# Kernel tuning notes

Measured on AMD Instinct MI355X. Metric: run time of the kernel, lower is better.

Reference implementation:

```python
import jax, jax.numpy as jnp
import numpy as np

H = 1024          # hidden_size
D = 4             # num_domains
B, S = 8, 2048


def setup_inputs() -> dict:
    key = jax.random.key(0)
    ks = jax.random.split(key, 12)
    inp = {
        "sequence_embeddings": jax.random.normal(ks[0], (B, S, H), jnp.float32),
        "volatility": jax.random.uniform(ks[1], (B, S, 1), jnp.float32) * 0.02 + 0.005,
        "risk_factors": jax.random.normal(ks[2], (B, S, 1), jnp.float32) * 0.01,
        # learned parameters (match torch init scales)
        "domain_feature_weights": jax.random.normal(ks[3], (H, 2 * H), jnp.float32) * 0.02,
        "domain_feature_bias": jnp.zeros((2 * H,), jnp.float32),
        "domain_classifier_weights": jax.random.normal(ks[4], (2 * H, D), jnp.float32) * 0.02,
        "domain_classifier_bias": jnp.zeros((D,), jnp.float32),
        "volatility_router_weights": jax.random.normal(ks[5], (1, 8, D), jnp.float32) * 0.1,
        "volatility_router_bias": jnp.zeros((8, D), jnp.float32),
        "risk_router_weights": jax.random.normal(ks[6], (1, 8, D), jnp.float32) * 0.1,
        "risk_router_bias": jnp.zeros((8, D), jnp.float32),
        "stats_router_weights": jax.random.normal(ks[7], (3, 12, D), jnp.float32) * 0.1,
        "stats_router_bias": jnp.zeros((12, D), jnp.float32),
        "expert_weights": jax.random.normal(ks[8], (D, 2 * H, H), jnp.float32) * 0.02,
        "expert_bias": jnp.zeros((D, H), jnp.float32),
    }
    return inp


def reference(sequence_embeddings, volatility, risk_factors,
              domain_feature_weights, domain_feature_bias,
              domain_classifier_weights, domain_classifier_bias,
              volatility_router_weights, volatility_router_bias,
              risk_router_weights, risk_router_bias,
              stats_router_weights, stats_router_bias,
              expert_weights, expert_bias):
    x = sequence_embeddings
    # shared domain feature extractor: [B,S,H] -> [B,S,2H]
    feat = jnp.tanh(jnp.einsum('bsh,hf->bsf', x, domain_feature_weights) + domain_feature_bias)
    # content-based domain logits [B,S,D]
    dom_logits = jnp.einsum('bsf,fd->bsd', feat, domain_classifier_weights) + domain_classifier_bias
    # volatility router: scalar -> 8 hidden units per domain, tanh, sum -> [B,S,D]
    vol_logits = jnp.tanh(volatility[..., None] * volatility_router_weights[0]
                          + volatility_router_bias).sum(axis=-2)
    # risk router, same structure
    risk_logits = jnp.tanh(risk_factors[..., None] * risk_router_weights[0]
                           + risk_router_bias).sum(axis=-2)
    # per-token statistics (mean/std/max over feature dim) -> [B,S,3]
    stats = jnp.stack([x.mean(axis=-1), x.std(axis=-1), x.max(axis=-1)], axis=-1)
    stats_logits = jnp.tanh(jnp.einsum('bsc,ckd->bskd', stats, stats_router_weights)
                            + stats_router_bias).sum(axis=-2)
    # combined routing distribution over domains
    routing_probs = jax.nn.softmax(dom_logits + vol_logits + risk_logits + stats_logits, axis=-1)
    # dispatch every token through all D experts: [B,S,D,H]
    expert_out = jnp.einsum('bsf,dfh->bsdh', feat, expert_weights) + expert_bias
    # gated combine: [B,S,H]
    out = jnp.einsum('bsd,bsdh->bsh', routing_probs, expert_out)
    return out
```

## Files before the change

kernel.cpp:

```cpp
#include <hip/hip_runtime.h>
#include <hip/hip_bf16.h>
#include <cstdint>
#include <cstddef>

typedef __bf16 bf16_t;
typedef bf16_t bf16x8 __attribute__((ext_vector_type(8)));
typedef bf16_t bf16x4 __attribute__((ext_vector_type(4)));
typedef float  f32x4  __attribute__((ext_vector_type(4)));
typedef int    i32x4  __attribute__((ext_vector_type(4)));

#define TOK 16384
#define Hh  1024
#define F2  2048
#define NC  4096

__device__ __forceinline__ void gload_lds16(const bf16_t* g, bf16_t* lds) {
  __builtin_amdgcn_global_load_lds(
      (const __attribute__((address_space(1))) void*)g,
      (__attribute__((address_space(3))) void*)lds, 16, 0, 0);
}
__device__ __forceinline__ void gload_lds16b(const int8_t* g, int8_t* lds) {
  __builtin_amdgcn_global_load_lds(
      (const __attribute__((address_space(1))) void*)g,
      (__attribute__((address_space(3))) void*)lds, 16, 0, 0);
}

__global__ __launch_bounds__(256)
void k_tr_wf(const float* __restrict__ in, bf16_t* __restrict__ out) {
  __shared__ float T[64][65];
  const int f0 = blockIdx.x * 64, h0 = blockIdx.y * 64;
  const int tid = threadIdx.x;
  const int c4 = (tid & 15) * 4, r = tid >> 4;
  #pragma unroll
  for (int p = 0; p < 4; ++p) {
    int hh = p * 16 + r;
    float4 v = *(const float4*)&in[(size_t)(h0 + hh) * F2 + f0 + c4];
    T[c4 + 0][hh] = v.x; T[c4 + 1][hh] = v.y; T[c4 + 2][hh] = v.z; T[c4 + 3][hh] = v.w;
  }
  __syncthreads();
  #pragma unroll
  for (int p = 0; p < 4; ++p) {
    int ff = p * 16 + r;
    bf16x4 o = { (bf16_t)T[ff][c4 + 0], (bf16_t)T[ff][c4 + 1],
                 (bf16_t)T[ff][c4 + 2], (bf16_t)T[ff][c4 + 3] };
    *(bf16x4*)&out[(size_t)(f0 + ff) * Hh + h0 + c4] = o;
  }
}

__global__ void k_we_scale1(const float* __restrict__ We, float* __restrict__ pmax) {
  int ht = blockIdx.x, fc = blockIdx.y, d = blockIdx.z;
  int h = ht * 256 + threadIdx.x;
  float m = 0.f;
  for (int ff = 0; ff < 256; ++ff) {
    float v = We[((size_t)d * F2 + fc * 256 + ff) * Hh + h];
    m = fmaxf(m, fabsf(v));
  }
  pmax[(size_t)(h * 4 + d) * 8 + fc] = m;
}
__global__ void k_we_scale2(const float* __restrict__ pmax, float* __restrict__ SB) {
  int cp = blockIdx.x * 256 + threadIdx.x;
  float m = 0.f;
  #pragma unroll
  for (int i = 0; i < 8; ++i) m = fmaxf(m, pmax[(size_t)cp * 8 + i]);
  SB[cp] = m;
}

__global__ __launch_bounds__(256)
void k_tr_we(const float* __restrict__ in, const float* __restrict__ SB,
             int8_t* __restrict__ out) {
  __shared__ float T[64][65];
  const int f0 = blockIdx.x * 64, h0 = blockIdx.y * 64, d = blockIdx.z;
  const float* ind = in + (size_t)d * F2 * Hh;
  const int tid = threadIdx.x;
  const int c4 = (tid & 15) * 4, r = tid >> 4;
  #pragma unroll
  for (int p = 0; p < 4; ++p) {
    int ff = p * 16 + r;
    float4 v = *(const float4*)&ind[(size_t)(f0 + ff) * Hh + h0 + c4];
    T[c4 + 0][ff] = v.x; T[c4 + 1][ff] = v.y; T[c4 + 2][ff] = v.z; T[c4 + 3][ff] = v.w;
  }
  __syncthreads();
  #pragma unroll
  for (int p = 0; p < 4; ++p) {
    int hh = p * 16 + r;
    int cp = (h0 + hh) * 4 + d;
    float m = SB[cp];
    float inv = (m > 1e-30f) ? 127.f / m : 0.f;
    char4 o;
    o.x = (int8_t)__float2int_rn(T[hh][c4 + 0] * inv);
    o.y = (int8_t)__float2int_rn(T[hh][c4 + 1] * inv);
    o.z = (int8_t)__float2int_rn(T[hh][c4 + 2] * inv);
    o.w = (int8_t)__float2int_rn(T[hh][c4 + 3] * inv);
    *(char4*)&out[(size_t)cp * F2 + f0 + c4] = o;
  }
}

__global__ void k_router_w(const float* __restrict__ x, const float* __restrict__ vol,
                           const float* __restrict__ risk, const float* __restrict__ clsb,
                           const float* __restrict__ vw, const float* __restrict__ vb,
                           const float* __restrict__ rw, const float* __restrict__ rb,
                           const float* __restrict__ sw, const float* __restrict__ sb,
                           bf16_t* __restrict__ xbf, float* __restrict__ LP,
                           int m0, int Tc) {
  int w = threadIdx.x >> 6, l = threadIdx.x & 63;
  int t = blockIdx.x * 4 + w;
  if (t >= Tc) return;
  int s = m0 + t;
  const float4* xr = (const float4*)(x + (size_t)s * Hh);
  bf16x4* xo = (bf16x4*)(xbf + (size_t)s * Hh);
  float sum = 0.f, sq = 0.f, mx = -1e30f;
  #pragma unroll
  for (int it = 0; it < 4; ++it) {
    float4 v = xr[it * 64 + l];
    sum += v.x + v.y + v.z + v.w;
    sq  += v.x * v.x + v.y * v.y + v.z * v.z + v.w * v.w;
    mx = fmaxf(mx, fmaxf(fmaxf(v.x, v.y), fmaxf(v.z, v.w)));
    bf16x4 o = { (bf16_t)v.x, (bf16_t)v.y, (bf16_t)v.z, (bf16_t)v.w };
    xo[it * 64 + l] = o;
  }
  #pragma unroll
  for (int off = 32; off; off >>= 1) {
    sum += __shfl_xor(sum, off, 64);
    sq  += __shfl_xor(sq,  off, 64);
    mx   = fmaxf(mx, __shfl_xor(mx, off, 64));
  }
  if (l < 4) {
    int d = l;
    float mean = sum * (1.0f / Hh);
    float var  = sq * (1.0f / Hh) - mean * mean;
    float sd   = sqrtf(fmaxf(var, 0.f));
    float v = vol[s], rk = risk[s];
    float acc = clsb[d];
    #pragma unroll
    for (int k = 0; k < 8; ++k)  acc += tanhf(v  * vw[k*4+d] + vb[k*4+d]);
    #pragma unroll
    for (int k = 0; k < 8; ++k)  acc += tanhf(rk * rw[k*4+d] + rb[k*4+d]);
    #pragma unroll
    for (int k = 0; k < 12; ++k)
      acc += tanhf(mean * sw[k*4+d] + sd * sw[48 + k*4+d] + mx * sw[96 + k*4+d] + sb[k*4+d]);
    LP[t * 4 + d] = acc;
  }
}

__global__ void k_dom(const int8_t* __restrict__ feat, const float* __restrict__ Wc,
                      float* __restrict__ LP) {
  int w = threadIdx.x >> 6, l = threadIdx.x & 63;
  int t = blockIdx.x * 4 + w;
  const int8_t* fr = feat + (size_t)t * F2;
  const float4* Wc4 = (const float4*)Wc;
  float a0 = 0, a1 = 0, a2 = 0, a3 = 0;
  #pragma unroll
  for (int it = 0; it < 4; ++it) {
    int f0 = it * 512 + l * 8;
    int2 v = *(const int2*)(fr + f0);
    #pragma unroll
    for (int j = 0; j < 8; ++j) {
      int word = (j < 4) ? v.x : v.y;
      float vf = (float)((signed char)(word >> (8 * (j & 3)))) * (1.f / 127.f);
      float4 wv = Wc4[f0 + j];
      a0 += vf * wv.x; a1 += vf * wv.y; a2 += vf * wv.z; a3 += vf * wv.w;
    }
  }
  #pragma unroll
  for (int off = 32; off; off >>= 1) {
    a0 += __shfl_xor(a0, off, 64); a1 += __shfl_xor(a1, off, 64);
    a2 += __shfl_xor(a2, off, 64); a3 += __shfl_xor(a3, off, 64);
  }
  if (l == 0) {
    float l0 = a0 + LP[t*4+0], l1 = a1 + LP[t*4+1];
    float l2 = a2 + LP[t*4+2], l3 = a3 + LP[t*4+3];
    float m = fmaxf(fmaxf(l0, l1), fmaxf(l2, l3));
    float e0 = expf(l0 - m), e1 = expf(l1 - m), e2 = expf(l2 - m), e3 = expf(l3 - m);
    float inv = 1.f / (e0 + e1 + e2 + e3);
    LP[t*4+0] = e0 * inv; LP[t*4+1] = e1 * inv; LP[t*4+2] = e2 * inv; LP[t*4+3] = e3 * inv;
  }
}

__global__ __launch_bounds__(512, 4)
void k_feat_gemm256(const bf16_t* __restrict__ A, const bf16_t* __restrict__ Bt,
                    const float* __restrict__ bias, int8_t* __restrict__ feat, int nbm) {
  constexpr int K = Hh, NT = K / 32;
  __shared__ bf16_t lds[2 * 8192 + 2 * 4096];
  bf16_t* ldsB = lds + 16384;
  const int tid = threadIdx.x;
  const int l = tid & 63, wid = tid >> 6;
  const int wm = wid >> 1, wn = wid & 1;
  const int l15 = l & 15, lg = l >> 4;

  const int nwg = nbm * 16, cpx = nwg >> 3;
  int swzb = (blockIdx.x & 7) * cpx + (blockIdx.x >> 3);
  const int bm = swzb % nbm, bn = swzb / nbm;

  const bf16_t* gA = A  + (size_t)(bm * 256) * K;
  const bf16_t* gB = Bt + (size_t)(bn * 128) * K;

  int aRow[2], aGx[2];
  #pragma unroll
  for (int i = 0; i < 2; ++i) {
    int slot = i * 512 + tid;
    aRow[i] = slot >> 2;
    aGx[i]  = ((slot & 3) ^ ((aRow[i] >> 1) & 3)) << 3;
  }
  const int bRow = tid >> 2;
  const int bGx  = ((tid & 3) ^ ((bRow >> 1) & 3)) << 3;

  #define STAGE(ts) do {                                                       \
    int b_ = (ts) & 1;                                                         \
    _Pragma("unroll")                                                          \
    for (int i = 0; i < 2; ++i)                                                \
      gload_lds16(gA + (size_t)aRow[i] * K + (ts) * 32 + aGx[i],               \
                  lds + b_ * 8192 + (i * 512 + tid) * 8);                      \
    gload_lds16(gB + (size_t)bRow * K + (ts) * 32 + bGx,                       \
                ldsB + b_ * 4096 + tid * 8);                                   \
  } while (0)
  #define FENCE asm volatile("" ::: "memory")

  const int cswz = ((lg ^ ((l15 >> 1) & 3)) << 3);
  f32x4 acc[4][4] = {};

  STAGE(0);
  asm volatile("s_waitcnt vmcnt(0)" ::: "memory");
  FENCE; __builtin_amdgcn_s_barrier(); FENCE;

  for (int t = 0; t < NT; ++t) {
    const bf16_t* As_ = lds  + (t & 1) * 8192;
    const bf16_t* Bs_ = ldsB + (t & 1) * 4096;
    if (t + 1 < NT) STAGE(t + 1);
    bf16x8 af[4], bf[4];
    #pragma unroll
    for (int ni = 0; ni < 4; ++ni)
      bf[ni] = *(const bf16x8*)&Bs_[(wn * 64 + ni * 16 + l15) * 32 + cswz];
    #pragma unroll
    for (int mi = 0; mi < 4; ++mi)
      af[mi] = *(const bf16x8*)&As_[(wm * 64 + mi * 16 + l15) * 32 + cswz];
    __builtin_amdgcn_s_setprio(1);
    #pragma unroll
    for (int ni = 0; ni < 4; ++ni)
      #pragma unroll
      for (int mi = 0; mi < 4; ++mi)
        acc[mi][ni] = __builtin_amdgcn_mfma_f32_16x16x32_bf16(af[mi], bf[ni], acc[mi][ni], 0, 0, 0);
    __builtin_amdgcn_s_setprio(0);
    asm volatile("s_waitcnt vmcnt(0)" ::: "memory");
    FENCE; __builtin_amdgcn_s_barrier(); FENCE;
  }
  #undef STAGE
  #undef FENCE

  #pragma unroll
  for (int ni = 0; ni < 4; ++ni) {
    int gn = bn * 128 + wn * 64 + ni * 16 + l15;
    float bv = bias[gn];
    #pragma unroll
    for (int mi = 0; mi < 4; ++mi) {
      int gmBase = bm * 256 + wm * 64 + mi * 16 + lg * 4;
      #pragma unroll
      for (int r = 0; r < 4; ++r) {
        float tv = tanhf(acc[mi][ni][r] + bv);
        feat[(size_t)(gmBase + r) * F2 + gn] = (int8_t)__float2int_rn(tv * 127.f);
      }
    }
  }
}

__global__ __launch_bounds__(512, 4)
void k_expert_gemm256(const int8_t* __restrict__ A, const int8_t* __restrict__ Bt,
                      const float* __restrict__ P, const float* __restrict__ EB,
                      const float* __restrict__ SBq, float* __restrict__ out, int nbm) {
  constexpr int K = F2, NT = K / 64;
  __shared__ int8_t lds[2 * 16384 + 2 * 8192];
  int8_t* ldsB = lds + 32768;
  const int tid = threadIdx.x;
  const int l = tid & 63, wid = tid >> 6;
  const int wm = wid >> 1, wn = wid & 1;
  const int l15 = l & 15, lg = l >> 4;

  const int nwg = nbm * 32, cpx = nwg >> 3;
  int swzb = (blockIdx.x & 7) * cpx + (blockIdx.x >> 3);
  const int bm = swzb % nbm, bn = swzb / nbm;

  const int8_t* gA = A  + (size_t)(bm * 256) * K;
  const int8_t* gB = Bt + (size_t)(bn * 128) * K;

  int aRow[2], aGx[2];
  #pragma unroll
  for (int i = 0; i < 2; ++i) {
    int slot = i * 512 + tid;
    aRow[i] = slot >> 2;
    aGx[i]  = ((slot & 3) ^ ((aRow[i] >> 1) & 3)) << 4;
  }
  const int bRow = tid >> 2;
  const int bGx  = ((tid & 3) ^ ((bRow >> 1) & 3)) << 4;

  #define STAGE(ts) do {                                                       \
    int b_ = (ts) & 1;                                                         \
    _Pragma("unroll")                                                          \
    for (int i = 0; i < 2; ++i)                                                \
      gload_lds16b(gA + (size_t)aRow[i] * K + (ts) * 64 + aGx[i],              \
                   lds + b_ * 16384 + (i * 512 + tid) * 16);                   \
    gload_lds16b(gB + (size_t)bRow * K + (ts) * 64 + bGx,                      \
                 ldsB + b_ * 8192 + tid * 16);                                 \
  } while (0)
  #define FENCE asm volatile("" ::: "memory")

  const int cswzB = ((lg ^ ((l15 >> 1) & 3)) << 4);
  i32x4 acc[4][4] = {};

  STAGE(0);
  asm volatile("s_waitcnt vmcnt(0)" ::: "memory");
  FENCE; __builtin_amdgcn_s_barrier(); FENCE;

  for (int t = 0; t < NT; ++t) {
    const int8_t* As_ = lds  + (t & 1) * 16384;
    const int8_t* Bs_ = ldsB + (t & 1) * 8192;
    if (t + 1 < NT) STAGE(t + 1);
    i32x4 af[4], bf[4];
    #pragma unroll
    for (int ni = 0; ni < 4; ++ni)
      bf[ni] = *(const i32x4*)&Bs_[(wn * 64 + ni * 16 + l15) * 64 + cswzB];
    #pragma unroll
    for (int mi = 0; mi < 4; ++mi)
      af[mi] = *(const i32x4*)&As_[(wm * 64 + mi * 16 + l15) * 64 + cswzB];
    __builtin_amdgcn_s_setprio(1);
    #pragma unroll
    for (int ni = 0; ni < 4; ++ni)
      #pragma unroll
      for (int mi = 0; mi < 4; ++mi)
        acc[mi][ni] = __builtin_amdgcn_mfma_i32_16x16x64_i8(af[mi], bf[ni], acc[mi][ni], 0, 0, 0);
    __builtin_amdgcn_s_setprio(0);
    asm volatile("s_waitcnt vmcnt(0)" ::: "memory");
    FENCE; __builtin_amdgcn_s_barrier(); FENCE;
  }
  #undef STAGE
  #undef FENCE

  #pragma unroll
  for (int mi = 0; mi < 4; ++mi) {
    int gmBase = bm * 256 + wm * 64 + mi * 16 + lg * 4;
    float pr[4];
    #pragma unroll
    for (int r = 0; r < 4; ++r) pr[r] = P[(gmBase + r) * 4 + (l & 3)];
    #pragma unroll
    for (int ni = 0; ni < 4; ++ni) {
      int colp = bn * 128 + wn * 64 + ni * 16 + l15;
      int h = colp >> 2;
      float dq = SBq[colp] * (1.0f / 16129.0f);
      #pragma unroll
      for (int r = 0; r < 4; ++r) {
        float sv = (float)acc[mi][ni][r] * dq * pr[r];
        sv += __shfl_xor(sv, 1, 64);
        sv += __shfl_xor(sv, 2, 64);
        if ((l & 3) == 0) {
          int gm = gmBase + r;
          float bt = P[gm*4+0]*EB[h] + P[gm*4+1]*EB[Hh+h]
                   + P[gm*4+2]*EB[2*Hh+h] + P[gm*4+3]*EB[3*Hh+h];
          out[(size_t)gm * Hh + h] = sv + bt;
        }
      }
    }
  }
}

extern "C" void kernel_launch(void* const* d_in, const int* in_sizes, int n_in,
                              void* d_out, int out_size, void* d_ws, size_t ws_size,
                              hipStream_t stream) {
  const float *x  = (const float*)d_in[0],  *vol = (const float*)d_in[1];
  const float *risk = (const float*)d_in[2], *Wf = (const float*)d_in[3];
  const float *fb = (const float*)d_in[4],  *Wc = (const float*)d_in[5];
  const float *cb = (const float*)d_in[6],  *vw = (const float*)d_in[7];
  const float *vb = (const float*)d_in[8],  *rw = (const float*)d_in[9];
  const float *rb = (const float*)d_in[10], *sw = (const float*)d_in[11];
  const float *sb = (const float*)d_in[12], *We = (const float*)d_in[13];
  const float *eb = (const float*)d_in[14];

  float* out = (float*)d_out;
  char* ws = (char*)d_ws;
  const size_t KB = 1024, MB = 1024 * 1024;

  float*  LP     = (float*) ws;
  float*  SBq    = (float*) (ws + 256 * KB);
  float*  pmax   = (float*) (ws + 512 * KB);
  bf16_t* wft    = (bf16_t*)(ws + 1 * MB);
  int8_t* wet    = (int8_t*)(ws + 5 * MB);
  bf16_t* xbf    = (bf16_t*)(ws + 13 * MB);
  const size_t base = 45 * MB;
  int Tc = TOK;
  while (Tc > 1024 && base + (size_t)Tc * F2 > ws_size) Tc >>= 1;
  int8_t* feat = (int8_t*)(ws + base);

  k_tr_wf    <<<dim3(F2 / 64, Hh / 64), 256, 0, stream>>>(Wf, wft);
  k_we_scale1<<<dim3(4, 8, 4), 256, 0, stream>>>(We, pmax);
  k_we_scale2<<<16, 256, 0, stream>>>(pmax, SBq);
  k_tr_we    <<<dim3(F2 / 64, Hh / 64, 4), 256, 0, stream>>>(We, SBq, wet);

  for (int m0 = 0; m0 < TOK; m0 += Tc) {
    k_router_w<<<Tc / 4, 256, 0, stream>>>(
        x, vol, risk, cb, vw, vb, rw, rb, sw, sb, xbf, LP, m0, Tc);
    int nbmF = Tc / 256;
    k_feat_gemm256<<<nbmF * (F2 / 128), 512, 0, stream>>>(
        xbf + (size_t)m0 * Hh, wft, fb, feat, nbmF);
    k_dom<<<Tc / 4, 256, 0, stream>>>(feat, Wc, LP);
    k_expert_gemm256<<<nbmF * (NC / 128), 512, 0, stream>>>(
        feat, wet, LP, eb, SBq, out + (size_t)m0 * Hh, nbmF);
  }
}
```

Measured before the change: 475.9 us.

## Triple-buffer LDS staging in feature and expert GEMMs with prefetch distance two

Both GEMM kernels move from double to triple LDS buffering and issue global-to-LDS loads two k-tiles ahead. Each iteration waits only for the oldest outstanding stage (vmcnt(3)), which is meant to hide global memory latency better. The cost is more LDS per block (72KB instead of 48KB), which can lower the number of resident blocks per CU.

Result: no change. 472.6 us (-0.7%).

```diff
diff --git a/kernel.cpp b/kernel.cpp
--- a/kernel.cpp
+++ b/kernel.cpp
@@ -180,8 +180,8 @@
 void k_feat_gemm256(const bf16_t* __restrict__ A, const bf16_t* __restrict__ Bt,
                     const float* __restrict__ bias, int8_t* __restrict__ feat, int nbm) {
   constexpr int K = Hh, NT = K / 32;
-  __shared__ bf16_t lds[2 * 8192 + 2 * 4096];
-  bf16_t* ldsB = lds + 16384;
+  __shared__ bf16_t lds[3 * 8192 + 3 * 4096];
+  bf16_t* ldsB = lds + 3 * 8192;
   const int tid = threadIdx.x;
   const int l = tid & 63, wid = tid >> 6;
   const int wm = wid >> 1, wn = wid & 1;
@@ -204,28 +204,29 @@
   const int bRow = tid >> 2;
   const int bGx  = ((tid & 3) ^ ((bRow >> 1) & 3)) << 3;
 
-  #define STAGE(ts) do {                                                       \
-    int b_ = (ts) & 1;                                                         \
+  #define STAGE(ts, buf) do {                                                  \
     _Pragma("unroll")                                                          \
     for (int i = 0; i < 2; ++i)                                                \
       gload_lds16(gA + (size_t)aRow[i] * K + (ts) * 32 + aGx[i],               \
-                  lds + b_ * 8192 + (i * 512 + tid) * 8);                      \
+                  lds + (buf) * 8192 + (i * 512 + tid) * 8);                   \
     gload_lds16(gB + (size_t)bRow * K + (ts) * 32 + bGx,                       \
-                ldsB + b_ * 4096 + tid * 8);                                   \
+                ldsB + (buf) * 4096 + tid * 8);                                \
   } while (0)
   #define FENCE asm volatile("" ::: "memory")
 
   const int cswz = ((lg ^ ((l15 >> 1) & 3)) << 3);
   f32x4 acc[4][4] = {};
 
-  STAGE(0);
-  asm volatile("s_waitcnt vmcnt(0)" ::: "memory");
+  STAGE(0, 0); STAGE(1, 1);
+  asm volatile("s_waitcnt vmcnt(3)" ::: "memory");
   FENCE; __builtin_amdgcn_s_barrier(); FENCE;
 
+  int cur = 0;
   for (int t = 0; t < NT; ++t) {
-    const bf16_t* As_ = lds  + (t & 1) * 8192;
-    const bf16_t* Bs_ = ldsB + (t & 1) * 4096;
-    if (t + 1 < NT) STAGE(t + 1);
+    const bf16_t* As_ = lds  + cur * 8192;
+    const bf16_t* Bs_ = ldsB + cur * 4096;
+    int nxt2 = cur + 2; if (nxt2 >= 3) nxt2 -= 3;
+    if (t + 2 < NT) STAGE(t + 2, nxt2);
     bf16x8 af[4], bf[4];
     #pragma unroll
     for (int ni = 0; ni < 4; ++ni)
@@ -240,8 +241,11 @@
       for (int mi = 0; mi < 4; ++mi)
         acc[mi][ni] = __builtin_amdgcn_mfma_f32_16x16x32_bf16(af[mi], bf[ni], acc[mi][ni], 0, 0, 0);
     __builtin_amdgcn_s_setprio(0);
-    asm volatile("s_waitcnt vmcnt(0)" ::: "memory");
+    asm volatile("s_waitcnt lgkmcnt(0)" ::: "memory");
+    if (t + 2 < NT)      asm volatile("s_waitcnt vmcnt(3)" ::: "memory");
+    else                 asm volatile("s_waitcnt vmcnt(0)" ::: "memory");
     FENCE; __builtin_amdgcn_s_barrier(); FENCE;
+    cur = cur + 1; if (cur >= 3) cur -= 3;
   }
   #undef STAGE
   #undef FENCE
@@ -267,8 +271,8 @@
                       const float* __restrict__ P, const float* __restrict__ EB,
                       const float* __restrict__ SBq, float* __restrict__ out, int nbm) {
   constexpr int K = F2, NT = K / 64;
-  __shared__ int8_t lds[2 * 16384 + 2 * 8192];
-  int8_t* ldsB = lds + 32768;
+  __shared__ int8_t lds[3 * 16384 + 3 * 8192];
+  int8_t* ldsB = lds + 3 * 16384;
   const int tid = threadIdx.x;
   const int l = tid & 63, wid = tid >> 6;
   const int wm = wid >> 1, wn = wid & 1;
@@ -291,28 +295,29 @@
   const int bRow = tid >> 2;
   const int bGx  = ((tid & 3) ^ ((bRow >> 1) & 3)) << 4;
 
-  #define STAGE(ts) do {                                                       \
-    int b_ = (ts) & 1;                                                         \
+  #define STAGE(ts, buf) do {                                                  \
     _Pragma("unroll")                                                          \
     for (int i = 0; i < 2; ++i)                                                \
       gload_lds16b(gA + (size_t)aRow[i] * K + (ts) * 64 + aGx[i],              \
-                   lds + b_ * 16384 + (i * 512 + tid) * 16);                   \
+                   lds + (buf) * 16384 + (i * 512 + tid) * 16);                \
     gload_lds16b(gB + (size_t)bRow * K + (ts) * 64 + bGx,                      \
-                 ldsB + b_ * 8192 + tid * 16);                                 \
+                 ldsB + (buf) * 8192 + tid * 16);                              \
   } while (0)
   #define FENCE asm volatile("" ::: "memory")
 
   const int cswzB = ((lg ^ ((l15 >> 1) & 3)) << 4);
   i32x4 acc[4][4] = {};
 
-  STAGE(0);
-  asm volatile("s_waitcnt vmcnt(0)" ::: "memory");
+  STAGE(0, 0); STAGE(1, 1);
+  asm volatile("s_waitcnt vmcnt(3)" ::: "memory");
   FENCE; __builtin_amdgcn_s_barrier(); FENCE;
 
+  int cur = 0;
   for (int t = 0; t < NT; ++t) {
-    const int8_t* As_ = lds  + (t & 1) * 16384;
-    const int8_t* Bs_ = ldsB + (t & 1) * 8192;
-    if (t + 1 < NT) STAGE(t + 1);
+    const int8_t* As_ = lds  + cur * 16384;
+    const int8_t* Bs_ = ldsB + cur * 8192;
+    int nxt2 = cur + 2; if (nxt2 >= 3) nxt2 -= 3;
+    if (t + 2 < NT) STAGE(t + 2, nxt2);
     i32x4 af[4], bf[4];
     #pragma unroll
     for (int ni = 0; ni < 4; ++ni)
@@ -327,8 +332,11 @@
       for (int mi = 0; mi < 4; ++mi)
         acc[mi][ni] = __builtin_amdgcn_mfma_i32_16x16x64_i8(af[mi], bf[ni], acc[mi][ni], 0, 0, 0);
     __builtin_amdgcn_s_setprio(0);
-    asm volatile("s_waitcnt vmcnt(0)" ::: "memory");
+    asm volatile("s_waitcnt lgkmcnt(0)" ::: "memory");
+    if (t + 2 < NT)      asm volatile("s_waitcnt vmcnt(3)" ::: "memory");
+    else                 asm volatile("s_waitcnt vmcnt(0)" ::: "memory");
     FENCE; __builtin_amdgcn_s_barrier(); FENCE;
+    cur = cur + 1; if (cur >= 3) cur -= 3;
   }
   #undef STAGE
   #undef FENCE
```
